# Kernel optimization log

Measured on AMD Instinct MI355X. Metric: run time of the kernel, lower is better.

Reference implementation:

```python
import jax, jax.numpy as jnp
import numpy as np

N = 100000   # total nodes
E = 1000000  # edges
D = 64       # input_dim
H = 128      # embed_dim


def setup_inputs() -> dict:
    key = jax.random.key(0)
    k1, k2, k3, k4 = jax.random.split(key, 4)
    nodes = jnp.arange(N, dtype=jnp.int32)
    features = jax.random.normal(k1, (N, D), dtype=jnp.float32)
    edge_index = jax.random.randint(k2, (2, E), 0, N, dtype=jnp.int32)
    # nn.Linear(2*D, H): weight [H, 2D], bias [H]
    W = jax.random.normal(k3, (H, 2 * D), dtype=jnp.float32) / np.sqrt(2 * D)
    b = jax.random.normal(k4, (H,), dtype=jnp.float32) * 0.01
    return {"nodes": nodes, "features": features, "edge_index": edge_index,
            "W": W, "b": b}


def reference(nodes, features, edge_index, W, b):
    src, dst = edge_index[0], edge_index[1]
    # gcn=False: neighbors are undirected (both src->dst and dst->src).
    # Mean aggregator over all neighbors (full-neighborhood mean).
    ones = jnp.ones((E,), dtype=features.dtype)
    neigh_sum = (jax.ops.segment_sum(features[dst], src, num_segments=N)
                 + jax.ops.segment_sum(features[src], dst, num_segments=N))
    deg = (jax.ops.segment_sum(ones, src, num_segments=N)
           + jax.ops.segment_sum(ones, dst, num_segments=N))
    neigh_mean = neigh_sum / jnp.maximum(deg, 1.0)[:, None]  # [N, D]
    self_feats = features[nodes]            # [B, D]
    neigh_feats = neigh_mean[nodes]         # [B, D]
    combined = jnp.concatenate([self_feats, neigh_feats], axis=1)  # [B, 2D]
    out = jax.nn.relu(combined @ W.T + b)   # [B, H]
    return out
```

## Files before the change

kernel.cpp:

```cpp
#include <hip/hip_runtime.h>
#include <hip/hip_bf16.h>


#define D_IN 64
#define H_OUT 128
#define CAP 64
#define CAP_L 61
#define NPB 32
#define BSHIFT 8
#define BUK_N 256
#define NBUK_MAX 512
#define PASSA_BLOCKS 256
#define PASSA_THREADS 512

typedef unsigned long long ull;
typedef unsigned short ushortt;
typedef unsigned char uchar;
typedef __attribute__((ext_vector_type(8))) short bf16x8;
typedef __attribute__((ext_vector_type(4))) float f32x4;
typedef __attribute__((ext_vector_type(2))) float f32x2;

__device__ __forceinline__ ushortt f2bf(float f) {
    __hip_bfloat16 h = __float2bfloat16(f);
    return *reinterpret_cast<ushortt*>(&h);
}
__device__ __forceinline__ float bf2f(ushortt u) {
    unsigned int x = ((unsigned int)u) << 16;
    return __uint_as_float(x);
}

__global__ __launch_bounds__(PASSA_THREADS) void prep_kernel(
    const int* __restrict__ ei,
    unsigned* __restrict__ gbuf,
    int* __restrict__ blkcnt,
    const float4* __restrict__ feat4,
    const float4* __restrict__ w4,
    ushortt* __restrict__ fb,
    uint2* __restrict__ fq,
    ushortt* __restrict__ Wb,
    int E, int nbuk, int scap, int chunk, int nfeat8, int nw8)
{
    const int t = threadIdx.x;

    if (blockIdx.x >= PASSA_BLOCKS) {
        int i = (blockIdx.x - PASSA_BLOCKS) * PASSA_THREADS + t;
        if (i < nfeat8) {
            float4 a = feat4[2 * i], b = feat4[2 * i + 1];
            bf16x8 o;
            o[0] = (short)f2bf(a.x); o[1] = (short)f2bf(a.y);
            o[2] = (short)f2bf(a.z); o[3] = (short)f2bf(a.w);
            o[4] = (short)f2bf(b.x); o[5] = (short)f2bf(b.y);
            o[6] = (short)f2bf(b.z); o[7] = (short)f2bf(b.w);
            *(bf16x8*)&fb[(size_t)i * 8] = o;
            unsigned lo = (unsigned)__builtin_amdgcn_cvt_pk_fp8_f32(a.x, a.y, 0, false);
            lo = (unsigned)__builtin_amdgcn_cvt_pk_fp8_f32(a.z, a.w, (int)lo, true);
            unsigned hi = (unsigned)__builtin_amdgcn_cvt_pk_fp8_f32(b.x, b.y, 0, false);
            hi = (unsigned)__builtin_amdgcn_cvt_pk_fp8_f32(b.z, b.w, (int)hi, true);
            uint2 q; q.x = lo; q.y = hi;
            fq[i] = q;
        } else {
            int j = i - nfeat8;
            if (j < nw8) {
                float4 a = w4[2 * j], b = w4[2 * j + 1];
                bf16x8 o;
                o[0] = (short)f2bf(a.x); o[1] = (short)f2bf(a.y);
                o[2] = (short)f2bf(a.z); o[3] = (short)f2bf(a.w);
                o[4] = (short)f2bf(b.x); o[5] = (short)f2bf(b.y);
                o[6] = (short)f2bf(b.z); o[7] = (short)f2bf(b.w);
                *(bf16x8*)&Wb[(size_t)j * 8] = o;
            }
        }
        return;
    }

    __shared__ int lcnt[NBUK_MAX];
    for (int i = t; i < nbuk; i += PASSA_THREADS) lcnt[i] = 0;
    __syncthreads();

    const int E2 = 2 * E;
    int lo = blockIdx.x * chunk;
    int hi = lo + chunk; if (hi > E2) hi = E2;

    for (int i = lo + t; i < hi; i += PASSA_THREADS) {
        int u = ei[i];
        int v = (i < E) ? ei[E + i] : ei[i - E];
        int b = u >> BSHIFT;
        unsigned pk = ((unsigned)v << BSHIFT) | (unsigned)(u & (BUK_N - 1));
        int p = atomicAdd(&lcnt[b], 1);
        if (p < scap) gbuf[((size_t)blockIdx.x * nbuk + b) * scap + p] = pk;
    }
    __syncthreads();
    for (int b = t; b < nbuk; b += PASSA_THREADS)
        blkcnt[blockIdx.x * nbuk + b] = lcnt[b];
}

__global__ __launch_bounds__(512) void adj_lds_kernel(
    const unsigned* __restrict__ gbuf,
    const int* __restrict__ blkcnt,
    const int* __restrict__ ei,
    int* __restrict__ cnt,
    int* __restrict__ adj,
    int N, int E, int nbuk, int scap)
{
    __shared__ unsigned adj_l[BUK_N * CAP_L];
    __shared__ int cnt_l[BUK_N];
    __shared__ int scnt_l[PASSA_BLOCKS];
    __shared__ int satf;

    const int b = blockIdx.x;
    const int t = threadIdx.x;

    if (t == 0) satf = 0;
    if (t < BUK_N) cnt_l[t] = 0;
    if (t < PASSA_BLOCKS) {
        int c = blkcnt[t * nbuk + b];
        scnt_l[t] = c;
        if (c > scap) satf = 1;
    }
    __syncthreads();

    if (satf) {
        const int E2 = 2 * E;
        for (int i = t; i < E2; i += 512) {
            int u = ei[i];
            if ((u >> BSHIFT) != b) continue;
            int v = (i < E) ? ei[E + i] : ei[i - E];
            int ul = u & (BUK_N - 1);
            int p  = atomicAdd(&cnt_l[ul], 1);
            if (p < CAP_L) adj_l[ul * CAP_L + p] = (unsigned)v;
        }
    } else {
        const int wv   = t >> 6;
        const int lane = t & 63;
        for (int seg = wv; seg < PASSA_BLOCKS; seg += 8) {
            int c = scnt_l[seg]; if (c > scap) c = scap;
            const unsigned* base = gbuf + ((size_t)seg * nbuk + b) * scap;
            for (int i = lane; i < c; i += 64) {
                unsigned e = base[i];
                int ul = e & (BUK_N - 1);
                int v  = (int)(e >> BSHIFT);
                int p  = atomicAdd(&cnt_l[ul], 1);
                if (p < CAP_L) adj_l[ul * CAP_L + p] = (unsigned)v;
            }
        }
    }
    __syncthreads();

    if (t < BUK_N) {
        int g = (b << BSHIFT) + t;
        if (g < N) {
            int c = cnt_l[t];
            cnt[g] = c;
            int cl = c < CAP_L ? c : CAP_L;
            int k4 = (cl + 3) >> 2;
            for (int s = 0; s < k4; ++s) {
                uint4 o;
                o.x = adj_l[t * CAP_L + 4 * s + 0];
                o.y = adj_l[t * CAP_L + 4 * s + 1];
                o.z = adj_l[t * CAP_L + 4 * s + 2];
                o.w = adj_l[t * CAP_L + 4 * s + 3];
                *(uint4*)&adj[(size_t)g * CAP + 4 * s] = o;
            }
        }
    }
}

__global__ __launch_bounds__(256) void build_adj_kernel(
    const int* __restrict__ ei,
    int* __restrict__ cnt,
    int* __restrict__ adj,
    int E)
{
    const int part   = blockIdx.x & 7;
    const int bloc   = blockIdx.x >> 3;
    const int nbp    = gridDim.x >> 3;
    const int stride = nbp * 256;
    const int E2     = 2 * E;

    for (int i = bloc * 256 + (int)threadIdx.x; i < E2; i += stride) {
        int u = ei[i];
        if (((u >> 4) & 7) != part) continue;
        int v = (i < E) ? ei[E + i] : ei[i - E];
        int p = atomicAdd(&cnt[u], 1);
        if (p < CAP_L) adj[u * CAP + p] = v;
    }
}

__global__ __launch_bounds__(256) void aggregate_fp8_kernel(
    const uchar* __restrict__ fq,
    const int* __restrict__ adj,
    const int* __restrict__ cnt,
    ushortt* __restrict__ meanb,
    int N)
{
    int wid  = (blockIdx.x * blockDim.x + threadIdx.x) >> 6;
    int lane = threadIdx.x & 63;
    if (wid >= N) return;

    const int oct = lane >> 3;
    const int ol  = lane & 7;

    int c = cnt[wid];
    int ids = 0;
    if (lane < 32) ids = adj[wid * CAP + lane];

    int cc = c < CAP_L ? c : CAP_L;
    if (__builtin_expect(cc > 32, 0)) {
        if (lane >= 32 && lane < cc) ids = adj[wid * CAP + lane];
    }

    const uchar* fqb = fq + ol * 8;

    uint2 u0 = {0u, 0u}, u1 = {0u, 0u}, u2 = {0u, 0u}, u3 = {0u, 0u};
    if (cc > 0) {
        int jj = oct;      int a = jj < cc; int id = __shfl(ids, a ? jj : 0);
        u0 = *(const uint2*)(fqb + (size_t)id * 64);
        if (!a) { u0.x = 0u; u0.y = 0u; }
    }
    if (cc > 8) {
        int jj = 8 + oct;  int a = jj < cc; int id = __shfl(ids, a ? jj : 0);
        u1 = *(const uint2*)(fqb + (size_t)id * 64);
        if (!a) { u1.x = 0u; u1.y = 0u; }
    }
    if (cc > 16) {
        int jj = 16 + oct; int a = jj < cc; int id = __shfl(ids, a ? jj : 0);
        u2 = *(const uint2*)(fqb + (size_t)id * 64);
        if (!a) { u2.x = 0u; u2.y = 0u; }
    }
    if (cc > 24) {
        int jj = 24 + oct; int a = jj < cc; int id = __shfl(ids, a ? jj : 0);
        u3 = *(const uint2*)(fqb + (size_t)id * 64);
        if (!a) { u3.x = 0u; u3.y = 0u; }
    }

    f32x2 s0 = {0.f, 0.f}, s1 = {0.f, 0.f}, s2 = {0.f, 0.f}, s3 = {0.f, 0.f};
#define DEC(u)                                                       \
    s0 += __builtin_amdgcn_cvt_pk_f32_fp8((int)(u).x, false);        \
    s1 += __builtin_amdgcn_cvt_pk_f32_fp8((int)(u).x, true);         \
    s2 += __builtin_amdgcn_cvt_pk_f32_fp8((int)(u).y, false);        \
    s3 += __builtin_amdgcn_cvt_pk_f32_fp8((int)(u).y, true);
    DEC(u0); DEC(u1); DEC(u2); DEC(u3);

    if (__builtin_expect(cc > 32, 0)) {
        for (int j = 32; j < cc; j += 8) {
            int jj = j + oct; int a = jj < cc; int id = __shfl(ids, a ? jj : 0);
            uint2 u = *(const uint2*)(fqb + (size_t)id * 64);
            if (!a) { u.x = 0u; u.y = 0u; }
            DEC(u);
        }
    }
#undef DEC

    f32x2 a0, a1;
    {
        f32x2 t0, t1, t2, t3;
        t0.x = __shfl_xor(s0.x, 8);  t0.y = __shfl_xor(s0.y, 8);
        t1.x = __shfl_xor(s1.x, 8);  t1.y = __shfl_xor(s1.y, 8);
        t2.x = __shfl_xor(s2.x, 8);  t2.y = __shfl_xor(s2.y, 8);
        t3.x = __shfl_xor(s3.x, 8);  t3.y = __shfl_xor(s3.y, 8);
        bool hi = (oct & 1);
        a0 = hi ? (s2 + t2) : (s0 + t0);
        a1 = hi ? (s3 + t3) : (s1 + t1);
    }
    f32x2 b0;
    {
        f32x2 t0, t1;
        t0.x = __shfl_xor(a0.x, 16); t0.y = __shfl_xor(a0.y, 16);
        t1.x = __shfl_xor(a1.x, 16); t1.y = __shfl_xor(a1.y, 16);
        bool hi = (oct & 2);
        b0 = hi ? (a1 + t1) : (a0 + t0);
    }
    float cf;
    {
        f32x2 tt; tt.x = __shfl_xor(b0.x, 32); tt.y = __shfl_xor(b0.y, 32);
        f32x2 ss = b0 + tt;
        cf = (oct & 4) ? ss.y : ss.x;
    }

    float r = 1.0f / fmaxf((float)c, 1.0f);
    int d = 8 * ol + 4 * (oct & 1) + (oct & 2) + ((oct >> 2) & 1);
    meanb[(size_t)wid * D_IN + d] = f2bf(cf * r);
}

__global__ __launch_bounds__(256) void aggregate_f32_kernel(
    const float* __restrict__ feat,
    const int* __restrict__ adj,
    const int* __restrict__ cnt,
    ushortt* __restrict__ meanb,
    int N)
{
    int wid  = (blockIdx.x * blockDim.x + threadIdx.x) >> 6;
    int lane = threadIdx.x & 63;
    if (wid >= N) return;

    int c  = cnt[wid];
    int cc = c < CAP_L ? c : CAP_L;
    int ids = adj[wid * CAP + lane];

    float sum = 0.0f;
    int j = 0;
    for (; j + 8 <= cc; j += 8) {
        int i0 = __shfl(ids, j + 0);
        int i1 = __shfl(ids, j + 1);
        int i2 = __shfl(ids, j + 2);
        int i3 = __shfl(ids, j + 3);
        int i4 = __shfl(ids, j + 4);
        int i5 = __shfl(ids, j + 5);
        int i6 = __shfl(ids, j + 6);
        int i7 = __shfl(ids, j + 7);
        float f0 = feat[i0 * D_IN + lane];
        float f1 = feat[i1 * D_IN + lane];
        float f2 = feat[i2 * D_IN + lane];
        float f3 = feat[i3 * D_IN + lane];
        float f4 = feat[i4 * D_IN + lane];
        float f5 = feat[i5 * D_IN + lane];
        float f6 = feat[i6 * D_IN + lane];
        float f7 = feat[i7 * D_IN + lane];
        sum += ((f0 + f1) + (f2 + f3)) + ((f4 + f5) + (f6 + f7));
    }
    for (; j < cc; ++j)
        sum += feat[__shfl(ids, j) * D_IN + lane];

    float m = sum / fmaxf((float)c, 1.0f);
    meanb[(size_t)wid * D_IN + lane] = f2bf(m);
}

__global__ __launch_bounds__(256) void gemm_mfma_kernel(
    const int* __restrict__ nodes,
    const ushortt* __restrict__ fb,
    const ushortt* __restrict__ meanb,
    const ushortt* __restrict__ Wb,
    const float* __restrict__ bias,
    float* __restrict__ out,
    int N)
{
    __shared__ ushortt w_lds[128 * 136];
    __shared__ int gnode[64];

    const int t  = threadIdx.x;
    const int n0 = blockIdx.x * 64;

    if (t < 64) {
        int idx = n0 + t;
        gnode[t] = nodes[idx < N ? idx : N - 1];
    }
    for (int i = t; i < 128 * 16; i += 256) {
        int row = i >> 4, seg = i & 15;
        *(bf16x8*)&w_lds[row * 136 + seg * 8] =
            *(const bf16x8*)&Wb[row * 128 + seg * 8];
    }
    __syncthreads();

    const int w    = t >> 6;
    const int lane = t & 63;
    const int l15  = lane & 15;
    const int quad = lane >> 4;

    const int g = gnode[w * 16 + l15];
    const bf16x8 a0 = *(const bf16x8*)&fb[(size_t)g * D_IN +  0 + quad * 8];
    const bf16x8 a1 = *(const bf16x8*)&fb[(size_t)g * D_IN + 32 + quad * 8];
    const bf16x8 a2 = *(const bf16x8*)&meanb[(size_t)g * D_IN +  0 + quad * 8];
    const bf16x8 a3 = *(const bf16x8*)&meanb[(size_t)g * D_IN + 32 + quad * 8];

    const int  out_row = n0 + w * 16 + l15;
    const bool valid   = out_row < N;

#pragma unroll
    for (int tile = 0; tile < 8; ++tile) {
        const int h0 = tile * 16;
        const ushortt* wrow = &w_lds[(h0 + l15) * 136];
        bf16x8 b0 = *(const bf16x8*)&wrow[ 0 + quad * 8];
        bf16x8 b1 = *(const bf16x8*)&wrow[32 + quad * 8];
        bf16x8 b2 = *(const bf16x8*)&wrow[64 + quad * 8];
        bf16x8 b3 = *(const bf16x8*)&wrow[96 + quad * 8];

        f32x4 acc = {0.f, 0.f, 0.f, 0.f};
        acc = __builtin_amdgcn_mfma_f32_16x16x32_bf16(b0, a0, acc, 0, 0, 0);
        acc = __builtin_amdgcn_mfma_f32_16x16x32_bf16(b1, a1, acc, 0, 0, 0);
        acc = __builtin_amdgcn_mfma_f32_16x16x32_bf16(b2, a2, acc, 0, 0, 0);
        acc = __builtin_amdgcn_mfma_f32_16x16x32_bf16(b3, a3, acc, 0, 0, 0);

        if (valid) {
            float4 bv = *(const float4*)&bias[h0 + quad * 4];
            float4 o;
            o.x = fmaxf(acc[0] + bv.x, 0.0f);
            o.y = fmaxf(acc[1] + bv.y, 0.0f);
            o.z = fmaxf(acc[2] + bv.z, 0.0f);
            o.w = fmaxf(acc[3] + bv.w, 0.0f);
            *(float4*)&out[(size_t)out_row * H_OUT + h0 + quad * 4] = o;
        }
    }
}

__global__ __launch_bounds__(256) void gemm_kernel(
    const int* __restrict__ nodes,
    const float* __restrict__ feat,
    const ushortt* __restrict__ meanb,
    const float* __restrict__ W,
    const float* __restrict__ bias,
    float* __restrict__ out,
    int N)
{
    __shared__ float w_lds[64 * 132];
    __shared__ float comb_self[NPB * 68];
    __shared__ float comb_mean[NPB * 68];
    __shared__ int   gnode[NPB];

    const int t  = threadIdx.x;
    const int n0 = blockIdx.x * NPB;

    if (t < NPB) {
        int idx = n0 + t;
        if (idx >= N) idx = N - 1;
        gnode[t] = nodes[idx];
    }
    __syncthreads();

    for (int i = t; i < NPB * 64; i += 256) {
        int n = i >> 6, d = i & 63;
        int g = gnode[n];
        comb_self[n * 68 + d] = feat[g * D_IN + d];
        comb_mean[n * 68 + d] = bf2f(meanb[(size_t)g * D_IN + d]);
    }
    for (int i = t; i < H_OUT * 64; i += 256) {
        int h = i >> 6, kk = i & 63;
        w_lds[kk * 132 + h] = W[h * (2 * D_IN) + kk];
    }
    __syncthreads();

    const int tx = t & 31;
    const int ty = t >> 5;
    const int h0 = tx * 4;
    const int nl = ty * 4;

    float acc[4][4];
#pragma unroll
    for (int j = 0; j < 4; j++)
#pragma unroll
        for (int i = 0; i < 4; i++) acc[j][i] = 0.0f;

    for (int kk = 0; kk < 64; kk += 4) {
        float4 wvv[4], cv[4];
#pragma unroll
        for (int i = 0; i < 4; i++)
            wvv[i] = *(const float4*)&w_lds[(kk + i) * 132 + h0];
#pragma unroll
        for (int j = 0; j < 4; j++)
            cv[j] = *(const float4*)&comb_self[(nl + j) * 68 + kk];
#pragma unroll
        for (int j = 0; j < 4; j++) {
            const float* c = (const float*)&cv[j];
#pragma unroll
            for (int i = 0; i < 4; i++) {
                const float* wp = (const float*)&wvv[i];
                acc[j][0] += wp[0] * c[i];
                acc[j][1] += wp[1] * c[i];
                acc[j][2] += wp[2] * c[i];
                acc[j][3] += wp[3] * c[i];
            }
        }
    }
    __syncthreads();

    for (int i = t; i < H_OUT * 64; i += 256) {
        int h = i >> 6, kk = i & 63;
        w_lds[kk * 132 + h] = W[h * (2 * D_IN) + 64 + kk];
    }
    __syncthreads();

    for (int kk = 0; kk < 64; kk += 4) {
        float4 wvv[4], cv[4];
#pragma unroll
        for (int i = 0; i < 4; i++)
            wvv[i] = *(const float4*)&w_lds[(kk + i) * 132 + h0];
#pragma unroll
        for (int j = 0; j < 4; j++)
            cv[j] = *(const float4*)&comb_mean[(nl + j) * 68 + kk];
#pragma unroll
        for (int j = 0; j < 4; j++) {
            const float* c = (const float*)&cv[j];
#pragma unroll
            for (int i = 0; i < 4; i++) {
                const float* wp = (const float*)&wvv[i];
                acc[j][0] += wp[0] * c[i];
                acc[j][1] += wp[1] * c[i];
                acc[j][2] += wp[2] * c[i];
                acc[j][3] += wp[3] * c[i];
            }
        }
    }

    float4 bv = *(const float4*)&bias[h0];
#pragma unroll
    for (int j = 0; j < 4; j++) {
        int n = n0 + nl + j;
        if (n >= N) continue;
        float4 o;
        o.x = fmaxf(acc[j][0] + bv.x, 0.0f);
        o.y = fmaxf(acc[j][1] + bv.y, 0.0f);
        o.z = fmaxf(acc[j][2] + bv.z, 0.0f);
        o.w = fmaxf(acc[j][3] + bv.w, 0.0f);
        *(float4*)&out[(size_t)n * H_OUT + h0] = o;
    }
}

extern "C" void kernel_launch(void* const* d_in, const int* in_sizes, int n_in,
                              void* d_out, int out_size, void* d_ws, size_t ws_size,
                              hipStream_t stream) {
    const int*   nodes = (const int*)d_in[0];
    const float* feat  = (const float*)d_in[1];
    const int*   ei    = (const int*)d_in[2];
    const float* W     = (const float*)d_in[3];
    const float* bias  = (const float*)d_in[4];
    float*       out   = (float*)d_out;

    const int N  = in_sizes[0];
    const int E  = in_sizes[2] / 2;
    const int E2 = 2 * E;

    const int nbuk  = (N + BUK_N - 1) >> BSHIFT;
    const int chunk = (E2 + PASSA_BLOCKS - 1) / PASSA_BLOCKS;
    double ex = (double)chunk * (double)BUK_N / (double)N;
    int scap = ((int)(ex + 9.0 * __builtin_sqrt(ex)) + 31) & ~15;
    if (scap < 64) scap = 64;

    char* base = (char*)d_ws;
    size_t off = 0;
    auto aln = [](size_t x) { return (x + 63) & ~(size_t)63; };
    int*     cnt    = (int*)(base + off);     off = aln(off + (size_t)N * 4);
    int*     adj    = (int*)(base + off);     off = aln(off + (size_t)N * CAP * 4);
    ushortt* meanb  = (ushortt*)(base + off); off = aln(off + (size_t)N * D_IN * 2);
    int*     blkcnt = (int*)(base + off);     off = aln(off + (size_t)PASSA_BLOCKS * NBUK_MAX * 4);
    ushortt* Wb     = (ushortt*)(base + off); off = aln(off + (size_t)H_OUT * 2 * D_IN * 2);
    ushortt* fb     = (ushortt*)(base + off); off = aln(off + (size_t)N * D_IN * 2);
    uchar*   fq     = (uchar*)(base + off);   off = aln(off + (size_t)N * D_IN);
    unsigned* gbuf  = (unsigned*)(base + off);
    const size_t total = off + (size_t)PASSA_BLOCKS * nbuk * scap * 4;

    const bool full = (N <= 131072) && (nbuk <= NBUK_MAX) && (ws_size >= total)
                   && ((N * D_IN) % 8 == 0);

    const int ablocks = (int)(((size_t)N * 64 + 255) / 256);

    if (full) {
        const int nfeat8 = N * D_IN / 8;
        const int nw8    = H_OUT * 2 * D_IN / 8;
        const int conv_blocks = (nfeat8 + nw8 + PASSA_THREADS - 1) / PASSA_THREADS;
        prep_kernel<<<PASSA_BLOCKS + conv_blocks, PASSA_THREADS, 0, stream>>>(
            ei, gbuf, blkcnt, (const float4*)feat, (const float4*)W,
            fb, (uint2*)fq, Wb, E, nbuk, scap, chunk, nfeat8, nw8);
        adj_lds_kernel<<<nbuk, 512, 0, stream>>>(gbuf, blkcnt, ei,
                                                 cnt, adj, N, E, nbuk, scap);
        aggregate_fp8_kernel<<<ablocks, 256, 0, stream>>>(fq, adj, cnt,
                                                          meanb, N);
        gemm_mfma_kernel<<<(N + 63) / 64, 256, 0, stream>>>(
            nodes, fb, meanb, Wb, bias, out, N);
    } else {
        hipMemsetAsync(cnt, 0, (size_t)N * sizeof(int), stream);
        build_adj_kernel<<<2048, 256, 0, stream>>>(ei, cnt, adj, E);
        aggregate_f32_kernel<<<ablocks, 256, 0, stream>>>(feat, adj, cnt,
                                                          meanb, N);
        gemm_kernel<<<(N + NPB - 1) / NPB, 256, 0, stream>>>(
            nodes, feat, meanb, W, bias, out, N);
    }
}
```

Before: 196.7 us.

## Fuse LDS adjacency build with fp8 neighbor aggregation in one kernel

Merges the bucketed adjacency-building kernel with the fp8 mean-aggregation kernel. Each 1024-thread block builds its 256 nodes' adjacency lists in LDS, then has 16 waves aggregate 16 nodes each, reading neighbor ids straight from LDS. This removes the global round trip for adj/cnt and one kernel launch. In exchange, only nbuk (~391) large blocks run the gather, which may lower occupancy and latency hiding compared with the separate one-wave-per-node launch.

```diff
diff --git a/kernel.cpp b/kernel.cpp
--- a/kernel.cpp
+++ b/kernel.cpp
@@ -94,12 +94,12 @@
         blkcnt[blockIdx.x * nbuk + b] = lcnt[b];
 }
 
-__global__ __launch_bounds__(512) void adj_lds_kernel(
+__global__ __launch_bounds__(1024) void adj_agg_kernel(
     const unsigned* __restrict__ gbuf,
     const int* __restrict__ blkcnt,
     const int* __restrict__ ei,
-    int* __restrict__ cnt,
-    int* __restrict__ adj,
+    const uchar* __restrict__ fq,
+    ushortt* __restrict__ meanb,
     int N, int E, int nbuk, int scap)
 {
     __shared__ unsigned adj_l[BUK_N * CAP_L];
@@ -119,9 +119,12 @@
     }
     __syncthreads();
 
+    const int wv   = t >> 6;
+    const int lane = t & 63;
+
     if (satf) {
         const int E2 = 2 * E;
-        for (int i = t; i < E2; i += 512) {
+        for (int i = t; i < E2; i += 1024) {
             int u = ei[i];
             if ((u >> BSHIFT) != b) continue;
             int v = (i < E) ? ei[E + i] : ei[i - E];
@@ -130,9 +133,7 @@
             if (p < CAP_L) adj_l[ul * CAP_L + p] = (unsigned)v;
         }
     } else {
-        const int wv   = t >> 6;
-        const int lane = t & 63;
-        for (int seg = wv; seg < PASSA_BLOCKS; seg += 8) {
+        for (int seg = wv; seg < PASSA_BLOCKS; seg += 16) {
             int c = scnt_l[seg]; if (c > scap) c = scap;
             const unsigned* base = gbuf + ((size_t)seg * nbuk + b) * scap;
             for (int i = lane; i < c; i += 64) {
@@ -146,22 +147,93 @@
     }
     __syncthreads();
 
-    if (t < BUK_N) {
-        int g = (b << BSHIFT) + t;
-        if (g < N) {
-            int c = cnt_l[t];
-            cnt[g] = c;
-            int cl = c < CAP_L ? c : CAP_L;
-            int k4 = (cl + 3) >> 2;
-            for (int s = 0; s < k4; ++s) {
-                uint4 o;
-                o.x = adj_l[t * CAP_L + 4 * s + 0];
-                o.y = adj_l[t * CAP_L + 4 * s + 1];
-                o.z = adj_l[t * CAP_L + 4 * s + 2];
-                o.w = adj_l[t * CAP_L + 4 * s + 3];
-                *(uint4*)&adj[(size_t)g * CAP + 4 * s] = o;
+    const int oct = lane >> 3;
+    const int ol  = lane & 7;
+    const uchar* fqb = fq + ol * 8;
+
+    for (int ni = 0; ni < 16; ++ni) {
+        const int n = wv * 16 + ni;
+        const int g = (b << BSHIFT) + n;
+        if (g >= N) break;
+
+        const int c  = cnt_l[n];
+        const int cc = c < CAP_L ? c : CAP_L;
+        const unsigned* arow = &adj_l[n * CAP_L];
+
+        uint2 u0 = {0u, 0u}, u1 = {0u, 0u}, u2 = {0u, 0u}, u3 = {0u, 0u};
+        if (cc > 0) {
+            int jj = oct;      int a = jj < cc;
+            unsigned id = arow[a ? jj : 0];
+            u0 = *(const uint2*)(fqb + (size_t)(id * 64u));
+            if (!a) { u0.x = 0u; u0.y = 0u; }
+        }
+        if (cc > 8) {
+            int jj = 8 + oct;  int a = jj < cc;
+            unsigned id = arow[a ? jj : 0];
+            u1 = *(const uint2*)(fqb + (size_t)(id * 64u));
+            if (!a) { u1.x = 0u; u1.y = 0u; }
+        }
+        if (cc > 16) {
+            int jj = 16 + oct; int a = jj < cc;
+            unsigned id = arow[a ? jj : 0];
+            u2 = *(const uint2*)(fqb + (size_t)(id * 64u));
+            if (!a) { u2.x = 0u; u2.y = 0u; }
+        }
+        if (cc > 24) {
+            int jj = 24 + oct; int a = jj < cc;
+            unsigned id = arow[a ? jj : 0];
+            u3 = *(const uint2*)(fqb + (size_t)(id * 64u));
+            if (!a) { u3.x = 0u; u3.y = 0u; }
+        }
+
+        f32x2 s0 = {0.f, 0.f}, s1 = {0.f, 0.f}, s2 = {0.f, 0.f}, s3 = {0.f, 0.f};
+#define DEC(u)                                                       \
+        s0 += __builtin_amdgcn_cvt_pk_f32_fp8((int)(u).x, false);    \
+        s1 += __builtin_amdgcn_cvt_pk_f32_fp8((int)(u).x, true);     \
+        s2 += __builtin_amdgcn_cvt_pk_f32_fp8((int)(u).y, false);    \
+        s3 += __builtin_amdgcn_cvt_pk_f32_fp8((int)(u).y, true);
+        DEC(u0); DEC(u1); DEC(u2); DEC(u3);
+
+        if (__builtin_expect(cc > 32, 0)) {
+            for (int j = 32; j < cc; j += 8) {
+                int jj = j + oct; int a = jj < cc;
+                unsigned id = arow[a ? jj : 0];
+                uint2 u = *(const uint2*)(fqb + (size_t)(id * 64u));
+                if (!a) { u.x = 0u; u.y = 0u; }
+                DEC(u);
             }
         }
+#undef DEC
+
+        f32x2 a0, a1;
+        {
+            f32x2 t0, t1, t2, t3;
+            t0.x = __shfl_xor(s0.x, 8);  t0.y = __shfl_xor(s0.y, 8);
+            t1.x = __shfl_xor(s1.x, 8);  t1.y = __shfl_xor(s1.y, 8);
+            t2.x = __shfl_xor(s2.x, 8);  t2.y = __shfl_xor(s2.y, 8);
+            t3.x = __shfl_xor(s3.x, 8);  t3.y = __shfl_xor(s3.y, 8);
+            bool hi = (oct & 1);
+            a0 = hi ? (s2 + t2) : (s0 + t0);
+            a1 = hi ? (s3 + t3) : (s1 + t1);
+        }
+        f32x2 b0;
+        {
+            f32x2 t0, t1;
+            t0.x = __shfl_xor(a0.x, 16); t0.y = __shfl_xor(a0.y, 16);
+            t1.x = __shfl_xor(a1.x, 16); t1.y = __shfl_xor(a1.y, 16);
+            bool hi = (oct & 2);
+            b0 = hi ? (a1 + t1) : (a0 + t0);
+        }
+        float cf;
+        {
+            f32x2 tt; tt.x = __shfl_xor(b0.x, 32); tt.y = __shfl_xor(b0.y, 32);
+            f32x2 ss = b0 + tt;
+            cf = (oct & 4) ? ss.y : ss.x;
+        }
+
+        float r = 1.0f / fmaxf((float)c, 1.0f);
+        int d = 8 * ol + 4 * (oct & 1) + (oct & 2) + ((oct >> 2) & 1);
+        meanb[(size_t)g * D_IN + d] = f2bf(cf * r);
     }
 }
 
@@ -184,102 +256,6 @@
         int p = atomicAdd(&cnt[u], 1);
         if (p < CAP_L) adj[u * CAP + p] = v;
     }
-}
-
-__global__ __launch_bounds__(256) void aggregate_fp8_kernel(
-    const uchar* __restrict__ fq,
-    const int* __restrict__ adj,
-    const int* __restrict__ cnt,
-    ushortt* __restrict__ meanb,
-    int N)
-{
-    int wid  = (blockIdx.x * blockDim.x + threadIdx.x) >> 6;
-    int lane = threadIdx.x & 63;
-    if (wid >= N) return;
-
-    const int oct = lane >> 3;
-    const int ol  = lane & 7;
-
-    int c = cnt[wid];
-    int ids = 0;
-    if (lane < 32) ids = adj[wid * CAP + lane];
-
-    int cc = c < CAP_L ? c : CAP_L;
-    if (__builtin_expect(cc > 32, 0)) {
-        if (lane >= 32 && lane < cc) ids = adj[wid * CAP + lane];
-    }
-
-    const uchar* fqb = fq + ol * 8;
-
-    uint2 u0 = {0u, 0u}, u1 = {0u, 0u}, u2 = {0u, 0u}, u3 = {0u, 0u};
-    if (cc > 0) {
-        int jj = oct;      int a = jj < cc; int id = __shfl(ids, a ? jj : 0);
-        u0 = *(const uint2*)(fqb + (size_t)id * 64);
-        if (!a) { u0.x = 0u; u0.y = 0u; }
-    }
-    if (cc > 8) {
-        int jj = 8 + oct;  int a = jj < cc; int id = __shfl(ids, a ? jj : 0);
-        u1 = *(const uint2*)(fqb + (size_t)id * 64);
-        if (!a) { u1.x = 0u; u1.y = 0u; }
-    }
-    if (cc > 16) {
-        int jj = 16 + oct; int a = jj < cc; int id = __shfl(ids, a ? jj : 0);
-        u2 = *(const uint2*)(fqb + (size_t)id * 64);
-        if (!a) { u2.x = 0u; u2.y = 0u; }
-    }
-    if (cc > 24) {
-        int jj = 24 + oct; int a = jj < cc; int id = __shfl(ids, a ? jj : 0);
-        u3 = *(const uint2*)(fqb + (size_t)id * 64);
-        if (!a) { u3.x = 0u; u3.y = 0u; }
-    }
-
-    f32x2 s0 = {0.f, 0.f}, s1 = {0.f, 0.f}, s2 = {0.f, 0.f}, s3 = {0.f, 0.f};
-#define DEC(u)                                                       \
-    s0 += __builtin_amdgcn_cvt_pk_f32_fp8((int)(u).x, false);        \
-    s1 += __builtin_amdgcn_cvt_pk_f32_fp8((int)(u).x, true);         \
-    s2 += __builtin_amdgcn_cvt_pk_f32_fp8((int)(u).y, false);        \
-    s3 += __builtin_amdgcn_cvt_pk_f32_fp8((int)(u).y, true);
-    DEC(u0); DEC(u1); DEC(u2); DEC(u3);
-
-    if (__builtin_expect(cc > 32, 0)) {
-        for (int j = 32; j < cc; j += 8) {
-            int jj = j + oct; int a = jj < cc; int id = __shfl(ids, a ? jj : 0);
-            uint2 u = *(const uint2*)(fqb + (size_t)id * 64);
-            if (!a) { u.x = 0u; u.y = 0u; }
-            DEC(u);
-        }
-    }
-#undef DEC
-
-    f32x2 a0, a1;
-    {
-        f32x2 t0, t1, t2, t3;
-        t0.x = __shfl_xor(s0.x, 8);  t0.y = __shfl_xor(s0.y, 8);
-        t1.x = __shfl_xor(s1.x, 8);  t1.y = __shfl_xor(s1.y, 8);
-        t2.x = __shfl_xor(s2.x, 8);  t2.y = __shfl_xor(s2.y, 8);
-        t3.x = __shfl_xor(s3.x, 8);  t3.y = __shfl_xor(s3.y, 8);
-        bool hi = (oct & 1);
-        a0 = hi ? (s2 + t2) : (s0 + t0);
-        a1 = hi ? (s3 + t3) : (s1 + t1);
-    }
-    f32x2 b0;
-    {
-        f32x2 t0, t1;
-        t0.x = __shfl_xor(a0.x, 16); t0.y = __shfl_xor(a0.y, 16);
-        t1.x = __shfl_xor(a1.x, 16); t1.y = __shfl_xor(a1.y, 16);
-        bool hi = (oct & 2);
-        b0 = hi ? (a1 + t1) : (a0 + t0);
-    }
-    float cf;
-    {
-        f32x2 tt; tt.x = __shfl_xor(b0.x, 32); tt.y = __shfl_xor(b0.y, 32);
-        f32x2 ss = b0 + tt;
-        cf = (oct & 4) ? ss.y : ss.x;
-    }
-
-    float r = 1.0f / fmaxf((float)c, 1.0f);
-    int d = 8 * ol + 4 * (oct & 1) + (oct & 2) + ((oct >> 2) & 1);
-    meanb[(size_t)wid * D_IN + d] = f2bf(cf * r);
 }
 
 __global__ __launch_bounds__(256) void aggregate_f32_kernel(
@@ -540,8 +516,6 @@
     const bool full = (N <= 131072) && (nbuk <= NBUK_MAX) && (ws_size >= total)
                    && ((N * D_IN) % 8 == 0);
 
-    const int ablocks = (int)(((size_t)N * 64 + 255) / 256);
-
     if (full) {
         const int nfeat8 = N * D_IN / 8;
         const int nw8    = H_OUT * 2 * D_IN / 8;
@@ -549,13 +523,12 @@
         prep_kernel<<<PASSA_BLOCKS + conv_blocks, PASSA_THREADS, 0, stream>>>(
             ei, gbuf, blkcnt, (const float4*)feat, (const float4*)W,
             fb, (uint2*)fq, Wb, E, nbuk, scap, chunk, nfeat8, nw8);
-        adj_lds_kernel<<<nbuk, 512, 0, stream>>>(gbuf, blkcnt, ei,
-                                                 cnt, adj, N, E, nbuk, scap);
-        aggregate_fp8_kernel<<<ablocks, 256, 0, stream>>>(fq, adj, cnt,
-                                                          meanb, N);
+        adj_agg_kernel<<<nbuk, 1024, 0, stream>>>(gbuf, blkcnt, ei, fq,
+                                                  meanb, N, E, nbuk, scap);
         gemm_mfma_kernel<<<(N + 63) / 64, 256, 0, stream>>>(
             nodes, fb, meanb, Wb, bias, out, N);
     } else {
+        const int ablocks = (int)(((size_t)N * 64 + 255) / 256);
         hipMemsetAsync(cnt, 0, (size_t)N * sizeof(int), stream);
         build_adj_kernel<<<2048, 256, 0, stream>>>(ei, cnt, adj, E);
         aggregate_f32_kernel<<<ablocks, 256, 0, stream>>>(feat, adj, cnt,
```

Result: faster. 169.6 us (-13.8%).
